# Optimization experiments

Measured on AMD Instinct MI355X. Metric: run time of the kernel, lower is better.

The kernel has to match this reference:

```python
import jax, jax.numpy as jnp
import numpy as np

PATCH = 3
ALPHA = 0.1


def unfold_patches(x, patch):
    """Equivalent of F.unfold(x, patch, padding=patch//2, stride=1).
    x: [B, C, H, W] -> [B, C*patch*patch, H*W].
    Note: the exact ordering of the patch-channel axis does not affect the
    downstream correlation matrix (it is summed over), so we use a simple
    shifted-view stacking.
    """
    B, C, H, W = x.shape
    p = patch // 2
    xp = jnp.pad(x, ((0, 0), (0, 0), (p, p), (p, p)))  # zero pad, like unfold
    views = [xp[:, :, i:i + H, j:j + W] for i in range(patch) for j in range(patch)]
    lf = jnp.concatenate(views, axis=1)  # [B, C*patch^2, H, W]
    return lf.reshape(B, C * patch * patch, H * W)


def setup_inputs() -> dict:
    key = jax.random.key(0)
    k1, k2 = jax.random.split(key)
    x_lab = jax.random.normal(k1, (4, 3, 64, 64), dtype=jnp.float32)
    feature = jax.random.normal(k2, (4, 64, 64, 64), dtype=jnp.float32)
    return {"x_lab": x_lab, "feature": feature}


def reference(x_lab, feature):
    # scale_factor=1 and feature already at (H, W): the torch interpolates are identity.
    B, _, H, W = x_lab.shape
    HW = H * W
    # ab channels as values: [B, HW, 2]
    x_ab = x_lab[:, 1:3].reshape(B, 2, HW).transpose(0, 2, 1)
    # local patch features: [B, C*9, HW]
    lf = unfold_patches(feature, PATCH)
    # full non-local correlation: [B, HW, HW]
    corr = jnp.einsum('bcm,bcn->bmn', lf, lf)
    attn = jax.nn.softmax(corr / ALPHA, axis=-1)
    # weighted average of ab values: [B, HW, 2]
    weighted_ab = jnp.einsum('bmn,bnc->bmc', attn, x_ab)
    return weighted_ab.transpose(0, 2, 1).reshape(B, 2, H, W)
```

## Files before the change

kernel.cpp:

```cpp
#include <hip/hip_runtime.h>
#include <math.h>


#define B_ 4
#define CH 64
#define H_ 64
#define W_ 64
#define SCALE2 14.426950408889634f
#define STRIPE 1056
#define ROWB (4 * STRIPE)
#define NRING 10

typedef __attribute__((ext_vector_type(4)))  unsigned int uint4v;
typedef __attribute__((ext_vector_type(16))) float f32x16;
typedef __attribute__((ext_vector_type(8)))  int int8v;

__device__ inline void glds16(const void* g, void* l) {
    __builtin_amdgcn_global_load_lds(
        (const __attribute__((address_space(1))) unsigned int*)g,
        (__attribute__((address_space(3))) unsigned int*)l, 16, 0, 0);
}

__device__ inline float dec_e4m3(unsigned u) {
    unsigned e = (u >> 3) & 15u, m = u & 7u;
    float v = e ? __uint_as_float(((e + 120u) << 23) | (m << 20))
                : (float)m * 0x1p-9f;
    return (u & 0x80u) ? -v : v;
}

__global__ __launch_bounds__(256) void feat_to_fp8(
    const float* __restrict__ feat, unsigned char* __restrict__ tf,
    float* __restrict__ n2)
{
    const int b = blockIdx.y, y = blockIdx.x, t = (int)threadIdx.x;
    __shared__ float ld[CH][W_ + 1];
    #pragma unroll
    for (int i = 0; i < 16; ++i) {
        int idx = i * 256 + t;
        int c = idx >> 6, x = idx & 63;
        ld[c][x] = feat[(((size_t)b * CH + c) * H_ + y) * W_ + x];
    }
    __syncthreads();
    const int x = t >> 2, g = t & 3;
    const int cbase = (g >> 1) * 32 + (g & 1) * 8;
    unsigned int wd[4];
    #pragma unroll
    for (int w4 = 0; w4 < 4; ++w4) {
        float f[4];
        #pragma unroll
        for (int e = 0; e < 4; ++e) {
            int j = w4 * 4 + e;
            f[e] = ld[cbase + ((j >> 3) << 4) + (j & 7)][x];
        }
        unsigned int wv = 0;
        wv = __builtin_amdgcn_cvt_pk_fp8_f32(f[0], f[1], wv, false);
        wv = __builtin_amdgcn_cvt_pk_fp8_f32(f[2], f[3], wv, true);
        wd[w4] = wv;
    }
    float s = 0.f;
    #pragma unroll
    for (int w4 = 0; w4 < 4; ++w4)
        #pragma unroll
        for (int e = 0; e < 4; ++e) {
            float d = dec_e4m3((wd[w4] >> (8 * e)) & 0xffu);
            s = fmaf(d, d, s);
        }
    s += __shfl_xor(s, 1);
    s += __shfl_xor(s, 2);
    if (g == 0) n2[((size_t)b * H_ + y) * W_ + x] = s;

    unsigned char* dst = tf + (((size_t)b * H_ + y) * W_ + x) * CH + g * 16;
    *(uint4v*)dst = (uint4v){wd[0], wd[1], wd[2], wd[3]};
}

#define MXMFMA(A, Bv, C) \
    __builtin_amdgcn_mfma_scale_f32_32x32x64_f8f6f4(A, Bv, C, 0, 0, 0, 0x7F, 0, 0x7F)

__global__ __launch_bounds__(512) void nlwa_fp8(
    const float* __restrict__ xlab,
    const unsigned char* __restrict__ tf,
    const float* __restrict__ n2,
    float* __restrict__ out)
{
    const int b = blockIdx.y, ym = blockIdx.x;
    const int tid = (int)threadIdx.x;
    const int w = tid >> 6, l = tid & 63;
    const int l31 = l & 31, h = l >> 5;
    const int zh = w >> 2;
    const int w4 = w & 3;
    const int mt = (w >> 1) & 1, nh = w & 1;
    const int lo = zh << 5;

    __shared__ __attribute__((aligned(16))) char smem[23 * ROWB];
    __shared__ float state[2][2][64][4];
    __shared__ float mref_lds[64];
    char* ring  = smem + zh * (NRING * ROWB);
    char* aslab = smem + 2 * NRING * ROWB;

    const unsigned char* tfb = tf + (size_t)b * H_ * W_ * CH;
    const float* aab = xlab + ((size_t)b * 3 + 1) * H_ * W_;
    const float* bab = xlab + ((size_t)b * 3 + 2) * H_ * W_;

    if (tid < 184) {
        int s23 = tid >> 3, rem = tid & 7;
        int which = rem >> 2, t = rem & 3;
        char* base = smem + s23 * ROWB;
        *(uint4v*)(base + t * STRIPE + (which ? 65 * 16 : 0)) = (uint4v){0,0,0,0};
    }
    #pragma unroll
    for (int i = 0; i < 2; ++i) ((float*)state)[i * 512 + tid] = 0.f;

    if (tid < 64) {
        const float* n2b = n2 + (size_t)b * H_ * W_;
        float s = 0.f;
        #pragma unroll
        for (int dy = -1; dy <= 1; ++dy) {
            int y = ym + dy;
            if ((unsigned)y < H_) {
                #pragma unroll
                for (int dx = -1; dx <= 1; ++dx) {
                    int x = tid + dx;
                    if ((unsigned)x < W_) s += n2b[y * W_ + x];
                }
            }
        }
        mref_lds[tid] = s * SCALE2;
    }

    auto stage = [&](char* slabBase, int y, int t) {
        char* dst = slabBase + t * STRIPE + 16;
        if ((unsigned)y < H_) {
            const unsigned char* gp = tfb + ((size_t)y * W_ + l) * CH + t * 16;
            glds16(gp, dst);
        } else {
            *(uint4v*)(dst + l * 16) = (uint4v){0, 0, 0, 0};
        }
    };

    if (zh == 0) {
        for (int tau = w4; tau < 36; tau += 4) {
            int r = tau >> 2, t = tau & 3;
            if (r < 6) {
                int y = lo - 1 + r;
                stage(ring + ((y + 1) % NRING) * ROWB, y, t);
            } else {
                int dy = r - 6;
                stage(aslab + dy * ROWB, ym + dy - 1, t);
            }
        }
    } else {
        for (int tau = w4; tau < 24; tau += 4) {
            int r = tau >> 2, t = tau & 3;
            int y = lo - 1 + r;
            stage(ring + ((y + 1) % NRING) * ROWB, y, t);
        }
    }

    const int xn = (nh << 5) + l31;
    const int xm = (mt << 5) + l31;
    const int soL = h * STRIPE;
    const int soH = (2 + h) * STRIPE;

    auto ld32 = [&](const char* slab, int off) -> int8v {
        uint4v r0 = *(const uint4v*)(slab + soL + off);
        uint4v r1 = *(const uint4v*)(slab + soH + off);
        int8v a;
        a[0] = r0[0]; a[1] = r0[1]; a[2] = r0[2]; a[3] = r0[3];
        a[4] = r1[0]; a[5] = r1[1]; a[6] = r1[2]; a[7] = r1[3];
        return a;
    };

    __syncthreads();

    int8v Areg0[3], Areg1[3], Areg2[3];
    #pragma unroll
    for (int dx = 0; dx < 3; ++dx) {
        const int oa = (xm + dx) * 16;
        Areg0[dx] = ld32(aslab + 0 * ROWB, oa);
        Areg1[dx] = ld32(aslab + 1 * ROWB, oa);
        Areg2[dx] = ld32(aslab + 2 * ROWB, oa);
    }

    float Mref[16];
    #pragma unroll
    for (int r = 0; r < 16; ++r)
        Mref[r] = mref_lds[(mt << 5) + (r & 3) + ((r >> 2) << 3) + (h << 2)];

    #pragma unroll 1
    for (int p = 0; p < 8; ++p) {
        const int y0 = lo + (p << 2);

        if (p < 7) {
            #pragma unroll
            for (int k = 0; k < 4; ++k) {
                int y = y0 + 5 + k;
                stage(ring + ((y + 1) % NRING) * ROWB, y, w4);
            }
        }

        #pragma unroll
        for (int s = 0; s < 2; ++s) {
            const int yb = y0 + (s << 1);

            f32x16 acc0, acc1;
            #pragma unroll
            for (int r = 0; r < 16; ++r) { acc0[r] = 0.f; acc1[r] = 0.f; }

            const char* rb[4];
            #pragma unroll
            for (int j2 = 0; j2 < 4; ++j2)
                rb[j2] = ring + ((yb + j2) % NRING) * ROWB;

            #pragma unroll
            for (int dx = 0; dx < 3; ++dx) {
                const int ob = (xn + dx) * 16;
                int8v Bb0 = ld32(rb[0], ob);
                int8v Bb1 = ld32(rb[1], ob);
                int8v Bb2 = ld32(rb[2], ob);
                int8v Bb3 = ld32(rb[3], ob);
                acc0 = MXMFMA(Areg0[dx], Bb0, acc0);
                acc0 = MXMFMA(Areg1[dx], Bb1, acc0);
                acc0 = MXMFMA(Areg2[dx], Bb2, acc0);
                acc1 = MXMFMA(Areg0[dx], Bb1, acc1);
                acc1 = MXMFMA(Areg1[dx], Bb2, acc1);
                acc1 = MXMFMA(Areg2[dx], Bb3, acc1);
            }

            #pragma unroll
            for (int j = 0; j < 2; ++j) {
                const f32x16& ac = (j == 0) ? acc0 : acc1;
                float v[16]; int upd = 0;
                #pragma unroll
                for (int r = 0; r < 16; ++r) {
                    v[r] = fmaf(ac[r], SCALE2, -Mref[r]);
                    upd |= (v[r] > -30.0f) ? 1 : 0;
                }
                if (__any(upd)) {
                    const int yn = yb + j;
                    float av = aab[yn * W_ + xn];
                    float bv = bab[yn * W_ + xn];
                    #pragma unroll
                    for (int r = 0; r < 16; ++r) {
                        float pp  = exp2f(fminf(v[r], 80.0f));
                        float w0c = pp * av;
                        float w1c = pp * bv;
                        #pragma unroll
                        for (int off = 16; off >= 1; off >>= 1) {
                            pp  += __shfl_xor(pp,  off);
                            w0c += __shfl_xor(w0c, off);
                            w1c += __shfl_xor(w1c, off);
                        }
                        if (l31 == 0) {
                            int m = (mt << 5) + (r & 3) + ((r >> 2) << 3) + (h << 2);
                            float* st = &state[zh][nh][m][0];
                            st[0] += pp; st[1] += w0c; st[2] += w1c;
                        }
                    }
                }
            }
        }
        __syncthreads();
    }

    if (tid < 64) {
        float Ssum = 0.f, w0 = 0.f, w1 = 0.f;
        #pragma unroll
        for (int z2 = 0; z2 < 2; ++z2)
            #pragma unroll
            for (int n2i = 0; n2i < 2; ++n2i) {
                Ssum += state[z2][n2i][tid][0];
                w0   += state[z2][n2i][tid][1];
                w1   += state[z2][n2i][tid][2];
            }
        float inv = 1.0f / Ssum;
        out[(((size_t)b * 2 + 0) * H_ + ym) * W_ + tid] = w0 * inv;
        out[(((size_t)b * 2 + 1) * H_ + ym) * W_ + tid] = w1 * inv;
    }
}

extern "C" void kernel_launch(void* const* d_in, const int* in_sizes, int n_in,
                              void* d_out, int out_size, void* d_ws, size_t ws_size,
                              hipStream_t stream) {
    const float* xlab = (const float*)d_in[0];
    const float* feat = (const float*)d_in[1];
    float* out = (float*)d_out;
    unsigned char* tf = (unsigned char*)d_ws;
    float* n2   = (float*)((char*)d_ws + (size_t)1024 * 1024);

    dim3 gridT(H_, B_);
    feat_to_fp8<<<gridT, 256, 0, stream>>>(feat, tf, n2);
    dim3 gridM(H_, B_);
    nlwa_fp8<<<gridM, 512, 0, stream>>>(xlab, tf, n2, out);
}
```

Baseline: 43.19 us.

## Give each wave a private LDS ring to remove block-wide barriers in main loop

Result: slower. 49.92 us (+15.6%).

```diff
diff --git a/kernel.cpp b/kernel.cpp
--- a/kernel.cpp
+++ b/kernel.cpp
@@ -7,9 +7,9 @@
 #define H_ 64
 #define W_ 64
 #define SCALE2 14.426950408889634f
-#define STRIPE 1056
-#define ROWB (4 * STRIPE)
-#define NRING 10
+#define SLOT 2176
+#define NRING 6
+#define WRING (NRING * SLOT)
 
 typedef __attribute__((ext_vector_type(4)))  unsigned int uint4v;
 typedef __attribute__((ext_vector_type(16))) float f32x16;
@@ -87,26 +87,18 @@
     const int w = tid >> 6, l = tid & 63;
     const int l31 = l & 31, h = l >> 5;
     const int zh = w >> 2;
-    const int w4 = w & 3;
     const int mt = (w >> 1) & 1, nh = w & 1;
     const int lo = zh << 5;
 
-    __shared__ __attribute__((aligned(16))) char smem[23 * ROWB];
+    __shared__ __attribute__((aligned(16))) char smem[8 * WRING];
     __shared__ float state[2][2][64][4];
     __shared__ float mref_lds[64];
-    char* ring  = smem + zh * (NRING * ROWB);
-    char* aslab = smem + 2 * NRING * ROWB;
+    char* wring = smem + w * WRING;
 
     const unsigned char* tfb = tf + (size_t)b * H_ * W_ * CH;
     const float* aab = xlab + ((size_t)b * 3 + 1) * H_ * W_;
     const float* bab = xlab + ((size_t)b * 3 + 2) * H_ * W_;
 
-    if (tid < 184) {
-        int s23 = tid >> 3, rem = tid & 7;
-        int which = rem >> 2, t = rem & 3;
-        char* base = smem + s23 * ROWB;
-        *(uint4v*)(base + t * STRIPE + (which ? 65 * 16 : 0)) = (uint4v){0,0,0,0};
-    }
     #pragma unroll
     for (int i = 0; i < 2; ++i) ((float*)state)[i * 512 + tid] = 0.f;
 
@@ -127,43 +119,27 @@
         mref_lds[tid] = s * SCALE2;
     }
 
-    auto stage = [&](char* slabBase, int y, int t) {
-        char* dst = slabBase + t * STRIPE + 16;
+    if (l < 48) {
+        int slot = l >> 3, s = (l >> 1) & 3, e = l & 1;
+        *(uint4v*)(wring + slot * SLOT + (s * 34 + (e ? 33 : 0)) * 16) =
+            (uint4v){0, 0, 0, 0};
+    }
+
+    auto stage_w = [&](char* slotp, int y, int s, int side) {
+        char* dstb = slotp + (s * 34 + 1 - side) * 16;
         if ((unsigned)y < H_) {
-            const unsigned char* gp = tfb + ((size_t)y * W_ + l) * CH + t * 16;
-            glds16(gp, dst);
+            if (l < 33)
+                glds16(tfb + ((size_t)y * W_ + side * 31 + l) * CH + s * 16, dstb);
         } else {
-            *(uint4v*)(dst + l * 16) = (uint4v){0, 0, 0, 0};
+            if (l < 33) *(uint4v*)(dstb + l * 16) = (uint4v){0, 0, 0, 0};
         }
     };
 
-    if (zh == 0) {
-        for (int tau = w4; tau < 36; tau += 4) {
-            int r = tau >> 2, t = tau & 3;
-            if (r < 6) {
-                int y = lo - 1 + r;
-                stage(ring + ((y + 1) % NRING) * ROWB, y, t);
-            } else {
-                int dy = r - 6;
-                stage(aslab + dy * ROWB, ym + dy - 1, t);
-            }
-        }
-    } else {
-        for (int tau = w4; tau < 24; tau += 4) {
-            int r = tau >> 2, t = tau & 3;
-            int y = lo - 1 + r;
-            stage(ring + ((y + 1) % NRING) * ROWB, y, t);
-        }
-    }
-
-    const int xn = (nh << 5) + l31;
-    const int xm = (mt << 5) + l31;
-    const int soL = h * STRIPE;
-    const int soH = (2 + h) * STRIPE;
-
-    auto ld32 = [&](const char* slab, int off) -> int8v {
-        uint4v r0 = *(const uint4v*)(slab + soL + off);
-        uint4v r1 = *(const uint4v*)(slab + soH + off);
+    const int pbL = (h * 34 + l31) * 16;
+    const int pbH = ((2 + h) * 34 + l31) * 16;
+    auto ld32w = [&](const char* slotp, int dx) -> int8v {
+        uint4v r0 = *(const uint4v*)(slotp + pbL + dx * 16);
+        uint4v r1 = *(const uint4v*)(slotp + pbH + dx * 16);
         int8v a;
         a[0] = r0[0]; a[1] = r0[1]; a[2] = r0[2]; a[3] = r0[3];
         a[4] = r1[0]; a[5] = r1[1]; a[6] = r1[2]; a[7] = r1[3];
@@ -172,95 +148,116 @@
 
     __syncthreads();
 
+    char* aslot = wring + 5 * SLOT;
     int8v Areg0[3], Areg1[3], Areg2[3];
     #pragma unroll
-    for (int dx = 0; dx < 3; ++dx) {
-        const int oa = (xm + dx) * 16;
-        Areg0[dx] = ld32(aslab + 0 * ROWB, oa);
-        Areg1[dx] = ld32(aslab + 1 * ROWB, oa);
-        Areg2[dx] = ld32(aslab + 2 * ROWB, oa);
-    }
+    for (int dyi = 0; dyi < 3; ++dyi) {
+        int y = ym + dyi - 1;
+        #pragma unroll
+        for (int s = 0; s < 4; ++s) stage_w(aslot, y, s, mt);
+        asm volatile("s_waitcnt vmcnt(0)" ::: "memory");
+        #pragma unroll
+        for (int dx = 0; dx < 3; ++dx) {
+            int8v vA = ld32w(aslot, dx);
+            if (dyi == 0) Areg0[dx] = vA;
+            else if (dyi == 1) Areg1[dx] = vA;
+            else Areg2[dx] = vA;
+        }
+        asm volatile("s_waitcnt lgkmcnt(0)" ::: "memory");
+    }
+    if (l < 4)
+        *(uint4v*)(aslot + (l * 34 + (nh ? 33 : 0)) * 16) = (uint4v){0,0,0,0};
 
     float Mref[16];
     #pragma unroll
     for (int r = 0; r < 16; ++r)
         Mref[r] = mref_lds[(mt << 5) + (r & 3) + ((r >> 2) << 3) + (h << 2)];
 
+    const int xn = (nh << 5) + l31;
+
+    #pragma unroll
+    for (int j = 0; j < 4; ++j) {
+        int y = lo - 1 + j;
+        char* slotp = wring + ((y + 6) % 6) * SLOT;
+        #pragma unroll
+        for (int s = 0; s < 4; ++s) stage_w(slotp, y, s, nh);
+    }
+
     #pragma unroll 1
-    for (int p = 0; p < 8; ++p) {
-        const int y0 = lo + (p << 2);
-
-        if (p < 7) {
-            #pragma unroll
-            for (int k = 0; k < 4; ++k) {
-                int y = y0 + 5 + k;
-                stage(ring + ((y + 1) % NRING) * ROWB, y, w4);
-            }
-        }
-
-        #pragma unroll
-        for (int s = 0; s < 2; ++s) {
-            const int yb = y0 + (s << 1);
-
-            f32x16 acc0, acc1;
-            #pragma unroll
-            for (int r = 0; r < 16; ++r) { acc0[r] = 0.f; acc1[r] = 0.f; }
-
-            const char* rb[4];
-            #pragma unroll
-            for (int j2 = 0; j2 < 4; ++j2)
-                rb[j2] = ring + ((yb + j2) % NRING) * ROWB;
-
-            #pragma unroll
-            for (int dx = 0; dx < 3; ++dx) {
-                const int ob = (xn + dx) * 16;
-                int8v Bb0 = ld32(rb[0], ob);
-                int8v Bb1 = ld32(rb[1], ob);
-                int8v Bb2 = ld32(rb[2], ob);
-                int8v Bb3 = ld32(rb[3], ob);
-                acc0 = MXMFMA(Areg0[dx], Bb0, acc0);
-                acc0 = MXMFMA(Areg1[dx], Bb1, acc0);
-                acc0 = MXMFMA(Areg2[dx], Bb2, acc0);
-                acc1 = MXMFMA(Areg0[dx], Bb1, acc1);
-                acc1 = MXMFMA(Areg1[dx], Bb2, acc1);
-                acc1 = MXMFMA(Areg2[dx], Bb3, acc1);
-            }
-
-            #pragma unroll
-            for (int j = 0; j < 2; ++j) {
-                const f32x16& ac = (j == 0) ? acc0 : acc1;
-                float v[16]; int upd = 0;
+    for (int sp = 0; sp < 16; ++sp) {
+        const int yb = lo + (sp << 1);
+
+        asm volatile("s_waitcnt vmcnt(0)" ::: "memory");
+
+        if (yb + 3 <= lo + 32) {
+            char* sp3 = wring + ((yb + 3) % 6) * SLOT;
+            #pragma unroll
+            for (int s = 0; s < 4; ++s) stage_w(sp3, yb + 3, s, nh);
+        }
+        if (yb + 4 <= lo + 32) {
+            char* sp4 = wring + ((yb + 4) % 6) * SLOT;
+            #pragma unroll
+            for (int s = 0; s < 4; ++s) stage_w(sp4, yb + 4, s, nh);
+        }
+
+        const char* rs0 = wring + ((yb - 1 + 6) % 6) * SLOT;
+        const char* rs1 = wring + ((yb     + 6) % 6) * SLOT;
+        const char* rs2 = wring + ((yb + 1) % 6) * SLOT;
+        const char* rs3 = wring + ((yb + 2) % 6) * SLOT;
+
+        f32x16 acc0, acc1;
+        #pragma unroll
+        for (int r = 0; r < 16; ++r) { acc0[r] = 0.f; acc1[r] = 0.f; }
+
+        #pragma unroll
+        for (int dx = 0; dx < 3; ++dx) {
+            int8v Bb0 = ld32w(rs0, dx);
+            int8v Bb1 = ld32w(rs1, dx);
+            int8v Bb2 = ld32w(rs2, dx);
+            int8v Bb3 = ld32w(rs3, dx);
+            acc0 = MXMFMA(Areg0[dx], Bb0, acc0);
+            acc0 = MXMFMA(Areg1[dx], Bb1, acc0);
+            acc0 = MXMFMA(Areg2[dx], Bb2, acc0);
+            acc1 = MXMFMA(Areg0[dx], Bb1, acc1);
+            acc1 = MXMFMA(Areg1[dx], Bb2, acc1);
+            acc1 = MXMFMA(Areg2[dx], Bb3, acc1);
+        }
+
+        #pragma unroll
+        for (int j = 0; j < 2; ++j) {
+            const f32x16& ac = (j == 0) ? acc0 : acc1;
+            float v[16]; int upd = 0;
+            #pragma unroll
+            for (int r = 0; r < 16; ++r) {
+                v[r] = fmaf(ac[r], SCALE2, -Mref[r]);
+                upd |= (v[r] > -30.0f) ? 1 : 0;
+            }
+            if (__any(upd)) {
+                const int yn = yb + j;
+                float av = aab[yn * W_ + xn];
+                float bv = bab[yn * W_ + xn];
                 #pragma unroll
                 for (int r = 0; r < 16; ++r) {
-                    v[r] = fmaf(ac[r], SCALE2, -Mref[r]);
-                    upd |= (v[r] > -30.0f) ? 1 : 0;
-                }
-                if (__any(upd)) {
-                    const int yn = yb + j;
-                    float av = aab[yn * W_ + xn];
-                    float bv = bab[yn * W_ + xn];
+                    float pp  = exp2f(fminf(v[r], 80.0f));
+                    float w0c = pp * av;
+                    float w1c = pp * bv;
                     #pragma unroll
-                    for (int r = 0; r < 16; ++r) {
-                        float pp  = exp2f(fminf(v[r], 80.0f));
-                        float w0c = pp * av;
-                        float w1c = pp * bv;
-                        #pragma unroll
-                        for (int off = 16; off >= 1; off >>= 1) {
-                            pp  += __shfl_xor(pp,  off);
-                            w0c += __shfl_xor(w0c, off);
-                            w1c += __shfl_xor(w1c, off);
-                        }
-                        if (l31 == 0) {
-                            int m = (mt << 5) + (r & 3) + ((r >> 2) << 3) + (h << 2);
-                            float* st = &state[zh][nh][m][0];
-                            st[0] += pp; st[1] += w0c; st[2] += w1c;
-                        }
+                    for (int off = 16; off >= 1; off >>= 1) {
+                        pp  += __shfl_xor(pp,  off);
+                        w0c += __shfl_xor(w0c, off);
+                        w1c += __shfl_xor(w1c, off);
+                    }
+                    if (l31 == 0) {
+                        int m = (mt << 5) + (r & 3) + ((r >> 2) << 3) + (h << 2);
+                        float* st = &state[zh][nh][m][0];
+                        st[0] += pp; st[1] += w0c; st[2] += w1c;
                     }
                 }
             }
         }
-        __syncthreads();
-    }
+    }
+
+    __syncthreads();
 
     if (tid < 64) {
         float Ssum = 0.f, w0 = 0.f, w1 = 0.f;
```
